# Kernel optimization log

Hardware: AMD Instinct MI355X
Metric: run time of the kernel (lower is better)

## Reference

```python
import jax, jax.numpy as jnp
import numpy as np

N_NODES = 100000
N_EDGES = 3200000
N_FEAT = 512
N_HID = 128
K = 10
ALPHA = 0.1


def setup_inputs() -> dict:
    key = jax.random.key(0)
    k0, k1, k2, k3 = jax.random.split(key, 4)
    x = jax.random.normal(k0, (N_NODES, N_FEAT), dtype=jnp.float32)
    edge_index = jax.random.randint(k1, (2, N_EDGES), 0, N_NODES, dtype=jnp.int32)
    # Linear params (PyTorch default init scale ~ 1/sqrt(fan_in))
    W1 = jax.random.normal(k2, (N_FEAT, N_HID), dtype=jnp.float32) / np.float32(np.sqrt(N_FEAT))
    b1 = jnp.zeros((N_HID,), dtype=jnp.float32)
    W2 = jax.random.normal(k3, (N_HID, N_HID), dtype=jnp.float32) / np.float32(np.sqrt(N_HID))
    b2 = jnp.zeros((N_HID,), dtype=jnp.float32)
    # PPR init of GPR coefficients: temp[k] = alpha*(1-alpha)^k, temp[K] = (1-alpha)^K
    temp = ALPHA * (1.0 - ALPHA) ** np.arange(K + 1)
    temp[-1] = (1.0 - ALPHA) ** K
    temp = jnp.asarray(temp, dtype=jnp.float32)
    return {"x": x, "edge_index": edge_index, "W1": W1, "b1": b1, "W2": W2, "b2": b2, "temp": temp}


def _gcn_norm(edge_index, num_nodes):
    # add self-loops with weight 1, then symmetric normalization D^-1/2 A D^-1/2
    loop = jnp.arange(num_nodes, dtype=edge_index.dtype)
    row = jnp.concatenate([edge_index[0], loop])
    col = jnp.concatenate([edge_index[1], loop])
    w = jnp.ones(row.shape[0], dtype=jnp.float32)
    deg = jax.ops.segment_sum(w, col, num_segments=num_nodes)
    dinv = jnp.where(deg > 0, jax.lax.rsqrt(deg), 0.0)
    norm = dinv[row] * w * dinv[col]
    return row, col, norm


def reference(x, edge_index, W1, b1, W2, b2, temp):
    n = x.shape[0]
    h = jax.nn.relu(x @ W1 + b1)  # lin1 + relu (dropout p=0 is identity)
    h = h @ W2 + b2               # lin2
    row, col, norm = _gcn_norm(edge_index, n)

    def step(carry, gamma):
        hk, acc = carry
        # propagate: gather x_j = hk[row], scale by norm, scatter-add to col
        hk = jax.ops.segment_sum(norm[:, None] * hk[row], col, num_segments=n)
        return (hk, acc + gamma * hk), None

    (_, hidden), _ = jax.lax.scan(step, (h, temp[0] * h), temp[1:])
    return hidden
```

## Files before the change

### kernel.cpp

```cpp
#include <hip/hip_runtime.h>
#include <hip/hip_fp16.h>

#define NN 100000
#define NE 3200000
#define NF 512
#define NH 128
#define NK 10
#define LDA 40

typedef unsigned int u32;
typedef _Float16 f16;
typedef f16 f16x4 __attribute__((ext_vector_type(4)));
typedef f16 f16x8 __attribute__((ext_vector_type(8)));
typedef float f32x4 __attribute__((ext_vector_type(4)));

__device__ __forceinline__ float2 up2(u32 v) {
  __half2 h = *reinterpret_cast<__half2*>(&v);
  return __half22float2(h);
}
__device__ __forceinline__ u32 pk2(float a, float b) {
  __half2 h = __floats2half2_rn(a, b);
  return *reinterpret_cast<u32*>(&h);
}


__global__ void count_kernel(const int* __restrict__ col, int* __restrict__ cnt) {
  int e = blockIdx.x * 256 + threadIdx.x;
  if (e < NE) atomicAdd(&cnt[col[e]], 1);
}

__global__ void dinv_kernel(const int* __restrict__ cnt, float* __restrict__ dinv) {
  int i = blockIdx.x * 256 + threadIdx.x;
  if (i < NN) dinv[i] = rsqrtf((float)(cnt[i] + 1));
}

__global__ __launch_bounds__(256) void bsum_kernel(const int* __restrict__ cnt,
                                                   int* __restrict__ bsum) {
  int b = blockIdx.x;
  int t = threadIdx.x;
  int base = b * 1024;
  int s = 0;
#pragma unroll
  for (int j = 0; j < 4; ++j) {
    int i = base + t + j * 256;
    if (i < NN) s += cnt[i];
  }
  for (int off = 32; off > 0; off >>= 1) s += __shfl_down(s, off);
  __shared__ int wsum[4];
  if ((t & 63) == 0) wsum[t >> 6] = s;
  __syncthreads();
  if (t == 0) bsum[b] = wsum[0] + wsum[1] + wsum[2] + wsum[3];
}

__global__ void scan98_kernel(const int* __restrict__ bsum, int* __restrict__ boff,
                              int* __restrict__ colptr) {
  __shared__ int buf[128];
  int t = threadIdx.x;
  int v = (t < 98) ? bsum[t] : 0;
  buf[t] = v;
  __syncthreads();
  for (int off = 1; off < 128; off <<= 1) {
    int a = (t >= off) ? buf[t - off] : 0;
    __syncthreads();
    buf[t] += a;
    __syncthreads();
  }
  if (t < 98) boff[t] = buf[t] - v;
  if (t == 97) colptr[NN] = buf[t];
}

__global__ __launch_bounds__(1024) void localscan_kernel(const int* __restrict__ cnt,
                                                         const int* __restrict__ boff,
                                                         int* __restrict__ colptr,
                                                         int* __restrict__ cursor) {
  __shared__ int buf[1024];
  int b = blockIdx.x;
  int t = threadIdx.x;
  int i = b * 1024 + t;
  int v = (i < NN) ? cnt[i] : 0;
  buf[t] = v;
  __syncthreads();
  for (int off = 1; off < 1024; off <<= 1) {
    int a = (t >= off) ? buf[t - off] : 0;
    __syncthreads();
    buf[t] += a;
    __syncthreads();
  }
  if (i < NN) {
    int e = boff[b] + buf[t] - v;
    colptr[i] = e;
    cursor[i] = e;
  }
}

__global__ void fill_kernel(const int* __restrict__ row, const int* __restrict__ col,
                            const float* __restrict__ dinv, int* __restrict__ cursor,
                            int2* __restrict__ epack) {
  int e = blockIdx.x * 256 + threadIdx.x;
  if (e >= NE) return;
  int r = row[e], c = col[e];
  int pos = atomicAdd(&cursor[c], 1);
  int2 p;
  p.x = r;
  p.y = __float_as_int(dinv[r] * dinv[c]);
  epack[pos] = p;
}


__global__ __launch_bounds__(256) void gemm1_kernel(
    const float* __restrict__ X, const float* __restrict__ W,
    const float* __restrict__ bias, u32* __restrict__ hout) {
  __shared__ f16 smem[16384];
  __shared__ float bias_s[NH];
  f16* As = smem;
  f16* Bs = smem + 128 * LDA;
  int tid = threadIdx.x;
  int wave = tid >> 6, lane = tid & 63;
  int quad = lane >> 4, l16 = lane & 15;
  int row0 = blockIdx.x * 128;
  if (tid < NH) bias_s[tid] = bias[tid];

  f32x4 acc[2][8];
#pragma unroll
  for (int t = 0; t < 2; ++t)
#pragma unroll
    for (int u = 0; u < 8; ++u) acc[t][u] = (f32x4){0.f, 0.f, 0.f, 0.f};

  for (int k0 = 0; k0 < NF; k0 += 32) {
#pragma unroll
    for (int i = 0; i < 4; ++i) {
      int slot = tid + i * 256;
      int r = slot >> 3, q4 = slot & 7;
      int grow = row0 + r;
      float4 v = make_float4(0.f, 0.f, 0.f, 0.f);
      if (grow < NN) v = *(const float4*)(X + (size_t)grow * NF + k0 + q4 * 4);
      f16x4 h;
      h[0] = (f16)v.x; h[1] = (f16)v.y; h[2] = (f16)v.z; h[3] = (f16)v.w;
      *(f16x4*)(As + r * LDA + q4 * 4) = h;
    }
#pragma unroll
    for (int i = 0; i < 4; ++i) {
      int slot = tid + i * 256;
      int n = slot & 127, k4 = slot >> 7;
      f16x4 h;
#pragma unroll
      for (int j = 0; j < 4; ++j) h[j] = (f16)W[(size_t)(k0 + k4 * 4 + j) * NH + n];
      *(f16x4*)(Bs + n * LDA + k4 * 4) = h;
    }
    __syncthreads();
    f16x8 a0 = *(f16x8*)(As + (wave * 32 + l16) * LDA + quad * 8);
    f16x8 a1 = *(f16x8*)(As + (wave * 32 + 16 + l16) * LDA + quad * 8);
#pragma unroll
    for (int u = 0; u < 8; ++u) {
      f16x8 b = *(f16x8*)(Bs + (u * 16 + l16) * LDA + quad * 8);
      acc[0][u] = __builtin_amdgcn_mfma_f32_16x16x32_f16(a0, b, acc[0][u], 0, 0, 0);
      acc[1][u] = __builtin_amdgcn_mfma_f32_16x16x32_f16(a1, b, acc[1][u], 0, 0, 0);
    }
    __syncthreads();
  }
#pragma unroll
  for (int t = 0; t < 2; ++t)
#pragma unroll
    for (int u = 0; u < 8; ++u)
#pragma unroll
      for (int r = 0; r < 4; ++r) {
        int row = wave * 32 + t * 16 + quad * 4 + r;
        int col = u * 16 + l16;
        float v = acc[t][u][r] + bias_s[col];
        smem[row * 128 + col] = (f16)fmaxf(v, 0.f);
      }
  __syncthreads();
  const u32* os = (const u32*)smem;
#pragma unroll
  for (int i = 0; i < 8; ++i) {
    int idx4 = tid + i * 256;
    int row = idx4 >> 4;
    int grow = row0 + row;
    if (grow < NN) {
      uint4 v = *(const uint4*)(os + idx4 * 4);
      *(uint4*)(hout + (size_t)grow * 64 + (idx4 * 4 & 63)) = v;
    }
  }
}

__global__ __launch_bounds__(256) void gemm2_kernel(
    const u32* __restrict__ Xh, const float* __restrict__ W,
    const float* __restrict__ bias, u32* __restrict__ hout) {
  __shared__ f16 smem[16384];
  __shared__ float bias_s[NH];
  f16* As = smem;
  f16* Bs = smem + 128 * LDA;
  int tid = threadIdx.x;
  int wave = tid >> 6, lane = tid & 63;
  int quad = lane >> 4, l16 = lane & 15;
  int row0 = blockIdx.x * 128;
  if (tid < NH) bias_s[tid] = bias[tid];

  f32x4 acc[2][8];
#pragma unroll
  for (int t = 0; t < 2; ++t)
#pragma unroll
    for (int u = 0; u < 8; ++u) acc[t][u] = (f32x4){0.f, 0.f, 0.f, 0.f};

  for (int k0 = 0; k0 < NH; k0 += 32) {
#pragma unroll
    for (int i = 0; i < 2; ++i) {
      int slot = tid + i * 256;
      int r = slot >> 2, q = slot & 3;
      int grow = row0 + r;
      uint4 v = make_uint4(0, 0, 0, 0);
      if (grow < NN) v = *(const uint4*)(Xh + (size_t)grow * 64 + (k0 >> 1) + q * 4);
      *(uint4*)(As + r * LDA + q * 8) = v;
    }
#pragma unroll
    for (int i = 0; i < 4; ++i) {
      int slot = tid + i * 256;
      int n = slot & 127, k4 = slot >> 7;
      f16x4 h;
#pragma unroll
      for (int j = 0; j < 4; ++j) h[j] = (f16)W[(size_t)(k0 + k4 * 4 + j) * NH + n];
      *(f16x4*)(Bs + n * LDA + k4 * 4) = h;
    }
    __syncthreads();
    f16x8 a0 = *(f16x8*)(As + (wave * 32 + l16) * LDA + quad * 8);
    f16x8 a1 = *(f16x8*)(As + (wave * 32 + 16 + l16) * LDA + quad * 8);
#pragma unroll
    for (int u = 0; u < 8; ++u) {
      f16x8 b = *(f16x8*)(Bs + (u * 16 + l16) * LDA + quad * 8);
      acc[0][u] = __builtin_amdgcn_mfma_f32_16x16x32_f16(a0, b, acc[0][u], 0, 0, 0);
      acc[1][u] = __builtin_amdgcn_mfma_f32_16x16x32_f16(a1, b, acc[1][u], 0, 0, 0);
    }
    __syncthreads();
  }
#pragma unroll
  for (int t = 0; t < 2; ++t)
#pragma unroll
    for (int u = 0; u < 8; ++u)
#pragma unroll
      for (int r = 0; r < 4; ++r) {
        int row = wave * 32 + t * 16 + quad * 4 + r;
        int col = u * 16 + l16;
        smem[row * 128 + col] = (f16)(acc[t][u][r] + bias_s[col]);
      }
  __syncthreads();
  const u32* os = (const u32*)smem;
#pragma unroll
  for (int i = 0; i < 8; ++i) {
    int idx4 = tid + i * 256;
    int row = idx4 >> 4;
    int grow = row0 + row;
    if (grow < NN) {
      uint4 v = *(const uint4*)(os + idx4 * 4);
      *(uint4*)(hout + (size_t)grow * 64 + (idx4 * 4 & 63)) = v;
    }
  }
}


__global__ __launch_bounds__(256) void prop_kernel(
    const u32* __restrict__ src, u32* __restrict__ dst,
    const float* __restrict__ dinv, const int* __restrict__ colptr,
    const int2* __restrict__ epack) {
  int wave = threadIdx.x >> 6;
  int lane = threadIdx.x & 63;
  int node = blockIdx.x * 4 + wave;
  if (node >= NN) return;
  int beg = colptr[node];
  int end = colptr[node + 1];
  float ax0 = 0.f, ay0 = 0.f, ax1 = 0.f, ay1 = 0.f;
  for (int base = beg; base < end; base += 64) {
    int idx = base + lane;
    int r = 0;
    float wgt = 0.f;
    if (idx < end) {
      int2 p = epack[idx];
      r = p.x;
      r = (r < 0) ? 0 : ((r >= NN) ? NN - 1 : r);
      wgt = __int_as_float(p.y);
    }
    int m = end - base;
    if (m > 64) m = 64;
    int j = 0;
    for (; j + 2 <= m; j += 2) {
      int rj0 = __shfl(r, j);
      float wj0 = __shfl(wgt, j);
      int rj1 = __shfl(r, j + 1);
      float wj1 = __shfl(wgt, j + 1);
      float2 v0 = up2(src[(size_t)rj0 * 64 + lane]);
      float2 v1 = up2(src[(size_t)rj1 * 64 + lane]);
      ax0 = fmaf(wj0, v0.x, ax0);
      ay0 = fmaf(wj0, v0.y, ay0);
      ax1 = fmaf(wj1, v1.x, ax1);
      ay1 = fmaf(wj1, v1.y, ay1);
    }
    if (j < m) {
      int rj = __shfl(r, j);
      float wj = __shfl(wgt, j);
      float2 v = up2(src[(size_t)rj * 64 + lane]);
      ax0 = fmaf(wj, v.x, ax0);
      ay0 = fmaf(wj, v.y, ay0);
    }
  }
  float ax = ax0 + ax1;
  float ay = ay0 + ay1;
  float di = dinv[node];
  float sw = di * di;
  float2 vs = up2(src[(size_t)node * 64 + lane]);
  ax = fmaf(sw, vs.x, ax);
  ay = fmaf(sw, vs.y, ay);
  dst[(size_t)node * 64 + lane] = pk2(ax, ay);
}


__global__ void sum6_kernel(const u32* __restrict__ b0, const u32* __restrict__ b1,
                            const u32* __restrict__ b2, const u32* __restrict__ b3,
                            const u32* __restrict__ b4, const u32* __restrict__ b5,
                            const float* __restrict__ temp, float* __restrict__ out) {
  int i = blockIdx.x * 256 + threadIdx.x;
  float2 s = make_float2(0.f, 0.f);
  float2 v;
  v = up2(b0[i]); s.x = fmaf(temp[0], v.x, s.x); s.y = fmaf(temp[0], v.y, s.y);
  v = up2(b1[i]); s.x = fmaf(temp[1], v.x, s.x); s.y = fmaf(temp[1], v.y, s.y);
  v = up2(b2[i]); s.x = fmaf(temp[2], v.x, s.x); s.y = fmaf(temp[2], v.y, s.y);
  v = up2(b3[i]); s.x = fmaf(temp[3], v.x, s.x); s.y = fmaf(temp[3], v.y, s.y);
  v = up2(b4[i]); s.x = fmaf(temp[4], v.x, s.x); s.y = fmaf(temp[4], v.y, s.y);
  v = up2(b5[i]); s.x = fmaf(temp[5], v.x, s.x); s.y = fmaf(temp[5], v.y, s.y);
  ((float2*)out)[i] = s;
}

__global__ void sum5_kernel(const u32* __restrict__ b0, const u32* __restrict__ b1,
                            const u32* __restrict__ b2, const u32* __restrict__ b3,
                            const u32* __restrict__ b4,
                            const float* __restrict__ temp, float* __restrict__ out) {
  int i = blockIdx.x * 256 + threadIdx.x;
  float2 s = ((float2*)out)[i];
  float2 v;
  v = up2(b0[i]); s.x = fmaf(temp[6], v.x, s.x); s.y = fmaf(temp[6], v.y, s.y);
  v = up2(b1[i]); s.x = fmaf(temp[7], v.x, s.x); s.y = fmaf(temp[7], v.y, s.y);
  v = up2(b2[i]); s.x = fmaf(temp[8], v.x, s.x); s.y = fmaf(temp[8], v.y, s.y);
  v = up2(b3[i]); s.x = fmaf(temp[9], v.x, s.x); s.y = fmaf(temp[9], v.y, s.y);
  v = up2(b4[i]); s.x = fmaf(temp[10], v.x, s.x); s.y = fmaf(temp[10], v.y, s.y);
  ((float2*)out)[i] = s;
}


extern "C" void kernel_launch(void* const* d_in, const int* in_sizes, int n_in,
                              void* d_out, int out_size, void* d_ws, size_t ws_size,
                              hipStream_t stream) {
  const float* x = (const float*)d_in[0];
  const int* erow_in = (const int*)d_in[1];
  const int* ecol_in = erow_in + NE;
  const float* W1 = (const float*)d_in[2];
  const float* b1 = (const float*)d_in[3];
  const float* W2 = (const float*)d_in[4];
  const float* b2 = (const float*)d_in[5];
  const float* temp = (const float*)d_in[6];

  char* w = (char*)d_ws;
  size_t o = 0;
  auto alloc = [&](size_t bytes) -> void* {
    void* p = w + o;
    o += (bytes + 255) & ~(size_t)255;
    return p;
  };
  int* cnt = (int*)alloc((size_t)NN * 4);
  int* colptr = (int*)alloc((size_t)(NN + 1) * 4);
  int* cursor = (int*)alloc((size_t)NN * 4);
  float* dinv = (float*)alloc((size_t)NN * 4);
  int* bsum = (int*)alloc(128 * 4);
  int* boff = (int*)alloc(128 * 4);
  int2* epack = (int2*)alloc((size_t)NE * 8);
  u32* bufA = (u32*)alloc((size_t)NN * 64 * 4);
  u32* B[5];
  for (int i = 0; i < 5; ++i) B[i] = (u32*)alloc((size_t)NN * 64 * 4);
  float* outp = (float*)d_out;
  (void)ws_size;

  hipMemsetAsync(cnt, 0, (size_t)NN * 4, stream);
  count_kernel<<<NE / 256, 256, 0, stream>>>(ecol_in, cnt);
  dinv_kernel<<<(NN + 255) / 256, 256, 0, stream>>>(cnt, dinv);
  bsum_kernel<<<98, 256, 0, stream>>>(cnt, bsum);
  scan98_kernel<<<1, 128, 0, stream>>>(bsum, boff, colptr);
  localscan_kernel<<<98, 1024, 0, stream>>>(cnt, boff, colptr, cursor);
  fill_kernel<<<NE / 256, 256, 0, stream>>>(erow_in, ecol_in, dinv, cursor, epack);

  int gblocks = (NN + 127) / 128;
  gemm1_kernel<<<gblocks, 256, 0, stream>>>(x, W1, b1, bufA);
  gemm2_kernel<<<gblocks, 256, 0, stream>>>(bufA, W2, b2, B[0]);

  int pblocks = (NN + 3) / 4;
  prop_kernel<<<pblocks, 256, 0, stream>>>(B[0], B[1], dinv, colptr, epack);
  prop_kernel<<<pblocks, 256, 0, stream>>>(B[1], B[2], dinv, colptr, epack);
  prop_kernel<<<pblocks, 256, 0, stream>>>(B[2], B[3], dinv, colptr, epack);
  prop_kernel<<<pblocks, 256, 0, stream>>>(B[3], B[4], dinv, colptr, epack);
  prop_kernel<<<pblocks, 256, 0, stream>>>(B[4], bufA, dinv, colptr, epack);
  sum6_kernel<<<NN * 64 / 256, 256, 0, stream>>>(B[0], B[1], B[2], B[3], B[4], bufA,
                                                 temp, outp);
  prop_kernel<<<pblocks, 256, 0, stream>>>(bufA, B[0], dinv, colptr, epack);
  prop_kernel<<<pblocks, 256, 0, stream>>>(B[0], B[1], dinv, colptr, epack);
  prop_kernel<<<pblocks, 256, 0, stream>>>(B[1], B[2], dinv, colptr, epack);
  prop_kernel<<<pblocks, 256, 0, stream>>>(B[2], B[3], dinv, colptr, epack);
  prop_kernel<<<pblocks, 256, 0, stream>>>(B[3], B[4], dinv, colptr, epack);
  sum5_kernel<<<NN * 64 / 256, 256, 0, stream>>>(B[0], B[1], B[2], B[3], B[4], temp,
                                                 outp);
}
```

Measured before the change: 1.950 ms.

## Vectorize propagation gathers to 16-byte loads and partition atomics by XCD residue

The propagation kernel now splits each wave into four 16-lane groups. Each group gathers a full 256-byte fp16 neighbor row with uint4 loads, so a wave processes four edges per step, and the partial sums are combined with cross-lane xor shuffles. The count and fill kernels are launched with 8x the blocks, and each block only handles destinations in one of 8 node ranges, apparently to keep atomics for a node range on one XCD/L2. The cost is that every block re-reads the column indices, and the shuffle reduction adds overhead for low-degree nodes.

```diff
diff --git a/kernel.cpp b/kernel.cpp
--- a/kernel.cpp
+++ b/kernel.cpp
@@ -25,8 +25,13 @@
 
 
 __global__ void count_kernel(const int* __restrict__ col, int* __restrict__ cnt) {
-  int e = blockIdx.x * 256 + threadIdx.x;
-  if (e < NE) atomicAdd(&cnt[col[e]], 1);
+  int chunk = blockIdx.x >> 3;
+  int res = blockIdx.x & 7;
+  int e = chunk * 256 + threadIdx.x;
+  if (e >= NE) return;
+  int c = col[e];
+  if ((int)((u32)c / 12500u) != res) return;
+  atomicAdd(&cnt[c], 1);
 }
 
 __global__ void dinv_kernel(const int* __restrict__ cnt, float* __restrict__ dinv) {
@@ -96,9 +101,13 @@
 __global__ void fill_kernel(const int* __restrict__ row, const int* __restrict__ col,
                             const float* __restrict__ dinv, int* __restrict__ cursor,
                             int2* __restrict__ epack) {
-  int e = blockIdx.x * 256 + threadIdx.x;
+  int chunk = blockIdx.x >> 3;
+  int res = blockIdx.x & 7;
+  int e = chunk * 256 + threadIdx.x;
   if (e >= NE) return;
-  int r = row[e], c = col[e];
+  int c = col[e];
+  if ((int)((u32)c / 12500u) != res) return;
+  int r = row[e];
   int pos = atomicAdd(&cursor[c], 1);
   int2 p;
   p.x = r;
@@ -263,11 +272,17 @@
     const int2* __restrict__ epack) {
   int wave = threadIdx.x >> 6;
   int lane = threadIdx.x & 63;
+  int g = lane >> 4;
+  int l = lane & 15;
   int node = blockIdx.x * 4 + wave;
   if (node >= NN) return;
   int beg = colptr[node];
   int end = colptr[node + 1];
-  float ax0 = 0.f, ay0 = 0.f, ax1 = 0.f, ay1 = 0.f;
+  const uint4* s4 = (const uint4*)src;
+  float acc[8];
+#pragma unroll
+  for (int i = 0; i < 8; ++i) acc[i] = 0.f;
+
   for (int base = beg; base < end; base += 64) {
     int idx = base + lane;
     int r = 0;
@@ -280,35 +295,72 @@
     }
     int m = end - base;
     if (m > 64) m = 64;
+    int full = m >> 2;
     int j = 0;
-    for (; j + 2 <= m; j += 2) {
-      int rj0 = __shfl(r, j);
-      float wj0 = __shfl(wgt, j);
-      int rj1 = __shfl(r, j + 1);
-      float wj1 = __shfl(wgt, j + 1);
-      float2 v0 = up2(src[(size_t)rj0 * 64 + lane]);
-      float2 v1 = up2(src[(size_t)rj1 * 64 + lane]);
-      ax0 = fmaf(wj0, v0.x, ax0);
-      ay0 = fmaf(wj0, v0.y, ay0);
-      ax1 = fmaf(wj1, v1.x, ax1);
-      ay1 = fmaf(wj1, v1.y, ay1);
-    }
-    if (j < m) {
-      int rj = __shfl(r, j);
-      float wj = __shfl(wgt, j);
-      float2 v = up2(src[(size_t)rj * 64 + lane]);
-      ax0 = fmaf(wj, v.x, ax0);
-      ay0 = fmaf(wj, v.y, ay0);
-    }
-  }
-  float ax = ax0 + ax1;
-  float ay = ay0 + ay1;
+    for (; j + 2 <= full; j += 2) {
+      int rj0 = __shfl(r, j * 4 + g);
+      float wj0 = __shfl(wgt, j * 4 + g);
+      int rj1 = __shfl(r, j * 4 + 4 + g);
+      float wj1 = __shfl(wgt, j * 4 + 4 + g);
+      uint4 v0 = s4[(size_t)rj0 * 16 + l];
+      uint4 v1 = s4[(size_t)rj1 * 16 + l];
+      float2 f;
+      f = up2(v0.x); acc[0] = fmaf(wj0, f.x, acc[0]); acc[1] = fmaf(wj0, f.y, acc[1]);
+      f = up2(v0.y); acc[2] = fmaf(wj0, f.x, acc[2]); acc[3] = fmaf(wj0, f.y, acc[3]);
+      f = up2(v0.z); acc[4] = fmaf(wj0, f.x, acc[4]); acc[5] = fmaf(wj0, f.y, acc[5]);
+      f = up2(v0.w); acc[6] = fmaf(wj0, f.x, acc[6]); acc[7] = fmaf(wj0, f.y, acc[7]);
+      f = up2(v1.x); acc[0] = fmaf(wj1, f.x, acc[0]); acc[1] = fmaf(wj1, f.y, acc[1]);
+      f = up2(v1.y); acc[2] = fmaf(wj1, f.x, acc[2]); acc[3] = fmaf(wj1, f.y, acc[3]);
+      f = up2(v1.z); acc[4] = fmaf(wj1, f.x, acc[4]); acc[5] = fmaf(wj1, f.y, acc[5]);
+      f = up2(v1.w); acc[6] = fmaf(wj1, f.x, acc[6]); acc[7] = fmaf(wj1, f.y, acc[7]);
+    }
+    if (j < full) {
+      int rj = __shfl(r, j * 4 + g);
+      float wj = __shfl(wgt, j * 4 + g);
+      uint4 v = s4[(size_t)rj * 16 + l];
+      float2 f;
+      f = up2(v.x); acc[0] = fmaf(wj, f.x, acc[0]); acc[1] = fmaf(wj, f.y, acc[1]);
+      f = up2(v.y); acc[2] = fmaf(wj, f.x, acc[2]); acc[3] = fmaf(wj, f.y, acc[3]);
+      f = up2(v.z); acc[4] = fmaf(wj, f.x, acc[4]); acc[5] = fmaf(wj, f.y, acc[5]);
+      f = up2(v.w); acc[6] = fmaf(wj, f.x, acc[6]); acc[7] = fmaf(wj, f.y, acc[7]);
+    }
+    int rem = m & 3;
+    if (rem) {
+      int rj = __shfl(r, full * 4 + g);
+      float wj = __shfl(wgt, full * 4 + g);
+      if (g < rem) {
+        uint4 v = s4[(size_t)rj * 16 + l];
+        float2 f;
+        f = up2(v.x); acc[0] = fmaf(wj, f.x, acc[0]); acc[1] = fmaf(wj, f.y, acc[1]);
+        f = up2(v.y); acc[2] = fmaf(wj, f.x, acc[2]); acc[3] = fmaf(wj, f.y, acc[3]);
+        f = up2(v.z); acc[4] = fmaf(wj, f.x, acc[4]); acc[5] = fmaf(wj, f.y, acc[5]);
+        f = up2(v.w); acc[6] = fmaf(wj, f.x, acc[6]); acc[7] = fmaf(wj, f.y, acc[7]);
+      }
+    }
+  }
   float di = dinv[node];
   float sw = di * di;
-  float2 vs = up2(src[(size_t)node * 64 + lane]);
-  ax = fmaf(sw, vs.x, ax);
-  ay = fmaf(sw, vs.y, ay);
-  dst[(size_t)node * 64 + lane] = pk2(ax, ay);
+  if (g == 0) {
+    uint4 v = s4[(size_t)node * 16 + l];
+    float2 f;
+    f = up2(v.x); acc[0] = fmaf(sw, f.x, acc[0]); acc[1] = fmaf(sw, f.y, acc[1]);
+    f = up2(v.y); acc[2] = fmaf(sw, f.x, acc[2]); acc[3] = fmaf(sw, f.y, acc[3]);
+    f = up2(v.z); acc[4] = fmaf(sw, f.x, acc[4]); acc[5] = fmaf(sw, f.y, acc[5]);
+    f = up2(v.w); acc[6] = fmaf(sw, f.x, acc[6]); acc[7] = fmaf(sw, f.y, acc[7]);
+  }
+#pragma unroll
+  for (int i = 0; i < 8; ++i) {
+    acc[i] += __shfl_xor(acc[i], 16);
+    acc[i] += __shfl_xor(acc[i], 32);
+  }
+  if (g == 0) {
+    uint4 o;
+    o.x = pk2(acc[0], acc[1]);
+    o.y = pk2(acc[2], acc[3]);
+    o.z = pk2(acc[4], acc[5]);
+    o.w = pk2(acc[6], acc[7]);
+    ((uint4*)dst)[(size_t)node * 16 + l] = o;
+  }
 }
 
 
@@ -377,12 +429,13 @@
   (void)ws_size;
 
   hipMemsetAsync(cnt, 0, (size_t)NN * 4, stream);
-  count_kernel<<<NE / 256, 256, 0, stream>>>(ecol_in, cnt);
+  count_kernel<<<(NE / 256) * 8, 256, 0, stream>>>(ecol_in, cnt);
   dinv_kernel<<<(NN + 255) / 256, 256, 0, stream>>>(cnt, dinv);
   bsum_kernel<<<98, 256, 0, stream>>>(cnt, bsum);
   scan98_kernel<<<1, 128, 0, stream>>>(bsum, boff, colptr);
   localscan_kernel<<<98, 1024, 0, stream>>>(cnt, boff, colptr, cursor);
-  fill_kernel<<<NE / 256, 256, 0, stream>>>(erow_in, ecol_in, dinv, cursor, epack);
+  fill_kernel<<<(NE / 256) * 8, 256, 0, stream>>>(erow_in, ecol_in, dinv, cursor,
+                                                  epack);
 
   int gblocks = (NN + 127) / 128;
   gemm1_kernel<<<gblocks, 256, 0, stream>>>(x, W1, b1, bufA);
```

Measured after the change: 1.787 ms. 8.3% less time.
